# Kernel tuning notes

Hardware: AMD Instinct MI355X
Metric: run time of the kernel (lower is better)

Reference implementation:

```python
import jax, jax.numpy as jnp
import numpy as np

NUM_HEADS = 32
NUM_KV_HEADS = 8
HEAD_DIM = 128
SCALE = 0.08838834764831845  # head_dim ** -0.5
LENS = [1024, 900, 800, 700, 600, 500, 400, 300]  # ragged sequence lengths


def setup_inputs() -> dict:
    key = jax.random.key(0)
    kq, kk, kv = jax.random.split(key, 3)
    cu = np.concatenate([[0], np.cumsum(LENS)]).astype(np.int32)
    T = int(cu[-1])  # 5224 total tokens
    q = jax.random.normal(kq, (T, NUM_HEADS * HEAD_DIM), jnp.float32)
    k = jax.random.normal(kk, (T, NUM_KV_HEADS * HEAD_DIM), jnp.float32)
    v = jax.random.normal(kv, (T, NUM_KV_HEADS * HEAD_DIM), jnp.float32)
    return {"q": q, "k": k, "v": v, "cu_seqlens": jnp.asarray(cu), "max_seqlen": 1024}


def _varlen_indices(cu_seqlens, total_tokens):
    # For each flat token, which sequence it belongs to and its position within it.
    pos = jnp.arange(total_tokens)
    seq_idx = jnp.searchsorted(cu_seqlens[1:], pos, side='right')
    pos_idx = pos - cu_seqlens[seq_idx]
    return seq_idx, pos_idx


def reference(q, k, v, cu_seqlens, max_seqlen):
    T = q.shape[0]
    B = cu_seqlens.shape[0] - 1
    q = q.reshape(T, NUM_HEADS, HEAD_DIM)
    k = k.reshape(T, NUM_KV_HEADS, HEAD_DIM)
    v = v.reshape(T, NUM_KV_HEADS, HEAD_DIM)
    si, pi = _varlen_indices(cu_seqlens, T)

    # varlen -> padded [B, L, H, D] (scatter)
    def pad(x):
        return jnp.zeros((B, max_seqlen) + x.shape[1:], x.dtype).at[si, pi].set(x)

    qp, kp, vp = pad(q), pad(k), pad(v)

    # GQA: repeat_interleave KV heads to match query heads
    rep = NUM_HEADS // NUM_KV_HEADS
    kp = jnp.repeat(kp, rep, axis=2)
    vp = jnp.repeat(vp, rep, axis=2)

    # causal SDPA on padded tensors
    scores = jnp.einsum('bihd,bjhd->bhij', qp, kp) * SCALE  # [B,H,L,L]
    causal = jnp.tril(jnp.ones((max_seqlen, max_seqlen), bool))
    scores = jnp.where(causal, scores, -jnp.inf)
    attn = jax.nn.softmax(scores, axis=-1)
    op = jnp.einsum('bhij,bjhd->bihd', attn, vp)  # [B,L,H,D]

    # padded -> varlen [T, H, D] (gather)
    return op[si, pi]
```

## Files before the change

### kernel.cpp

```cpp
#include <hip/hip_runtime.h>
#include <math.h>

#define NUM_HEADS 32
#define NUM_KV_HEADS 8
#define HEAD_DIM 128
#define QSTRIDE 4096
#define KSTRIDE 1024
#define SCALE 0.08838834764831845f
#define BM 128
#define PSP 72
#define K1C (SCALE * 1.4426950408889634f)
#define K2C (6.0f * 1.4426950408889634f)

typedef __attribute__((ext_vector_type(8))) short short8;
typedef __attribute__((ext_vector_type(16))) float floatx16;
typedef __attribute__((ext_vector_type(4))) float f32x4;

__constant__ unsigned char PERM41[41] = {
  7, 15, 6, 14, 21, 5, 13, 20, 26, 31, 4, 12, 19, 25, 35, 30,
  3, 11, 18, 24, 34, 38, 29, 2, 10, 17, 23, 33, 37, 40, 28,
  1, 9, 16, 22, 32, 36, 39, 27, 0, 8};

__device__ __forceinline__ ushort f2bf(float f) {
  union { float f; unsigned u; } x; x.f = f;
  unsigned r = x.u + 0x7fffu + ((x.u >> 16) & 1u);
  return (ushort)(r >> 16);
}

__device__ __forceinline__ unsigned cvtpk(float lo, float hi) {
  unsigned r;
  asm("v_cvt_pk_bf16_f32 %0, %1, %2" : "=v"(r) : "v"(lo), "v"(hi));
  return r;
}

__global__ __launch_bounds__(256)
void prep(const float* __restrict__ k, const float* __restrict__ v,
          ushort* __restrict__ kfr, ushort* __restrict__ vfr,
          int T, int NB32, int NB16) {
  const int kt = (int)blockIdx.x * 64;
  const int kvh = (int)blockIdx.y;
  __shared__ __align__(16) ushort Kt[64][136];
  __shared__ __align__(16) ushort Vs[128][PSP];
  {
    const int key = threadIdx.x >> 2;
    const int dc = (threadIdx.x & 3) * 32;
    const bool inb = (kt + key) < T;
    const float* gk = k + (size_t)(kt + key) * KSTRIDE + kvh * HEAD_DIM + dc;
    const float* gv = v + (size_t)(kt + key) * KSTRIDE + kvh * HEAD_DIM + dc;
    #pragma unroll
    for (int i = 0; i < 32; i += 8) {
      float4 a = inb ? *(const float4*)(gk + i) : make_float4(0.f, 0.f, 0.f, 0.f);
      float4 b = inb ? *(const float4*)(gk + i + 4) : make_float4(0.f, 0.f, 0.f, 0.f);
      ushort w[8] = {f2bf(a.x), f2bf(a.y), f2bf(a.z), f2bf(a.w),
                     f2bf(b.x), f2bf(b.y), f2bf(b.z), f2bf(b.w)};
      *(short8*)&Kt[key][dc + i] = *(short8*)w;
    }
    #pragma unroll
    for (int i = 0; i < 32; i += 4) {
      float4 x = inb ? *(const float4*)(gv + i) : make_float4(0.f, 0.f, 0.f, 0.f);
      Vs[dc + i + 0][key] = f2bf(x.x);
      Vs[dc + i + 1][key] = f2bf(x.y);
      Vs[dc + i + 2][key] = f2bf(x.z);
      Vs[dc + i + 3][key] = f2bf(x.w);
    }
  }
  __syncthreads();
  const int l = threadIdx.x & 63;
  const int wv = threadIdx.x >> 6;
  const int l32 = l & 31;
  const int hb = l >> 5;
  #pragma unroll
  for (int q0 = 0; q0 < 4; q0++) {
    int c = q0 * 4 + wv;
    int kb2 = c >> 3, s = c & 7;
    short8 d = *(const short8*)&Kt[kb2 * 32 + l32][s * 16 + hb * 8];
    *(short8*)(kfr + ((size_t)(kvh * NB32 + (kt >> 5) + kb2) * 8 + s) * 512 + l * 8) = d;
  }
  #pragma unroll
  for (int q0 = 0; q0 < 4; q0++) {
    int c = q0 * 4 + wv;
    int kb = c >> 2, i = c & 3;
    short8 d = *(const short8*)&Vs[i * 32 + l32][kb * 16 + hb * 8];
    *(short8*)(vfr + ((size_t)(kvh * NB16 + (kt >> 4) + kb) * 4 + i) * 512 + l * 8) = d;
  }
}

__global__ __launch_bounds__(256, 2)
void fa_kernel(const float* __restrict__ q, const ushort* __restrict__ kfr,
               const ushort* __restrict__ vfr, const int* __restrict__ cu,
               float* __restrict__ out, int T, int NB32, int NB16, int B, int nt) {
  const int tid = threadIdx.x;
  const int wave = tid >> 6;
  const int lane = tid & 63;
  const int l32 = lane & 31;
  const int half = lane >> 5;
  const int h = ((int)blockIdx.x & 7) * 4 + ((int)blockIdx.x >> 3);
  const int kvh = h >> 2;
  const int tile = (nt == 41) ? (int)PERM41[blockIdx.y] : (nt - 1 - (int)blockIdx.y);
  const int row0 = tile * BM;
  const int wrow0 = row0 + wave * 32;
  const int myrow = wrow0 + l32;

  int rs_q = 0, tk_q = -1;
  if (myrow < T) {
    int s = 0;
    while (s < B - 1 && cu[s + 1] <= myrow) s++;
    rs_q = cu[s]; tk_q = myrow;
  }
  const int wkt0 = (__shfl(rs_q, 0, 64) / 32) * 32;
  const int wtmax = (wrow0 < T) ? min(wrow0 + 31, T - 1) : -1;

  short8 aq[8];
  if (myrow < T) {
    const float* gq = q + (size_t)myrow * QSTRIDE + h * HEAD_DIM + half * 8;
    #pragma unroll
    for (int s = 0; s < 8; s++) {
      f32x4 x = __builtin_nontemporal_load((const f32x4*)(gq + s * 16));
      f32x4 y = __builtin_nontemporal_load((const f32x4*)(gq + s * 16 + 4));
      ushort w[8] = {f2bf(x.x), f2bf(x.y), f2bf(x.z), f2bf(x.w),
                     f2bf(y.x), f2bf(y.y), f2bf(y.z), f2bf(y.w)};
      aq[s] = *(short8*)w;
    }
  } else {
    #pragma unroll
    for (int s = 0; s < 8; s++) aq[s] = (short8){0, 0, 0, 0, 0, 0, 0, 0};
  }

  const ushort* kp = kfr + (size_t)kvh * NB32 * 4096 + (size_t)(wkt0 >> 5) * 4096 + lane * 8;
  const ushort* vp = vfr + (size_t)kvh * NB16 * 2048 + (size_t)(wkt0 >> 4) * 2048 + lane * 8;

  short8 kf[8], vf[8];
  #pragma unroll
  for (int s = 0; s < 8; s++) kf[s] = *(const short8*)(kp + s * 512);
  #pragma unroll
  for (int c = 0; c < 8; c++) vf[c] = *(const short8*)(vp + c * 512);

  floatx16 o0 = {0.f,0.f,0.f,0.f,0.f,0.f,0.f,0.f,0.f,0.f,0.f,0.f,0.f,0.f,0.f,0.f};
  floatx16 o1 = o0, o2 = o0, o3 = o0;
  float sm = 0.f;

  for (int kt = wkt0; kt <= wtmax; kt += 32) {
    floatx16 ca = {0.f,0.f,0.f,0.f,0.f,0.f,0.f,0.f,0.f,0.f,0.f,0.f,0.f,0.f,0.f,0.f};
    floatx16 cb = ca;
    __builtin_amdgcn_s_setprio(1);
    #pragma unroll
    for (int s = 0; s < 8; s += 2) {
      ca = __builtin_amdgcn_mfma_f32_32x32x16_bf16(kf[s], aq[s], ca, 0, 0, 0);
      cb = __builtin_amdgcn_mfma_f32_32x32x16_bf16(kf[s + 1], aq[s + 1], cb, 0, 0, 0);
    }
    __builtin_amdgcn_s_setprio(0);

    const bool more = (kt + 32) <= wtmax;
    kp += more ? 4096 : 0;
    #pragma unroll
    for (int s = 0; s < 8; s++) kf[s] = *(const short8*)(kp + s * 512);

    const bool fullt = __all((rs_q <= kt) & (tk_q >= kt + 31));
    if (fullt) {
      #pragma unroll
      for (int r = 0; r < 16; r++) {
        ca[r] = __builtin_amdgcn_exp2f(fmaf(ca[r] + cb[r], K1C, -K2C));
        sm += ca[r];
      }
    } else {
      #pragma unroll
      for (int r = 0; r < 16; r++) {
        int key = kt + (r & 3) + 8 * (r >> 2) + 4 * half;
        bool vld = (key >= rs_q) & (key <= tk_q);
        ca[r] = vld ? __builtin_amdgcn_exp2f(fmaf(ca[r] + cb[r], K1C, -K2C)) : 0.f;
        sm += ca[r];
      }
    }

    #pragma unroll
    for (int g = 0; g < 2; g++) {
      const int r0 = g * 8;
      unsigned w0 = cvtpk(ca[r0 + 0], ca[r0 + 1]);
      unsigned w1 = cvtpk(ca[r0 + 2], ca[r0 + 3]);
      unsigned w2 = cvtpk(ca[r0 + 4], ca[r0 + 5]);
      unsigned w3 = cvtpk(ca[r0 + 6], ca[r0 + 7]);
      asm("v_permlane32_swap_b32 %0, %1" : "+v"(w0), "+v"(w2));
      asm("v_permlane32_swap_b32 %0, %1" : "+v"(w1), "+v"(w3));
      union { unsigned u[4]; short8 s8; } ap;
      ap.u[0] = w0; ap.u[1] = w1; ap.u[2] = w2; ap.u[3] = w3;
      o0 = __builtin_amdgcn_mfma_f32_32x32x16_bf16(ap.s8, vf[g * 4 + 0], o0, 0, 0, 0);
      o1 = __builtin_amdgcn_mfma_f32_32x32x16_bf16(ap.s8, vf[g * 4 + 1], o1, 0, 0, 0);
      o2 = __builtin_amdgcn_mfma_f32_32x32x16_bf16(ap.s8, vf[g * 4 + 2], o2, 0, 0, 0);
      o3 = __builtin_amdgcn_mfma_f32_32x32x16_bf16(ap.s8, vf[g * 4 + 3], o3, 0, 0, 0);
    }

    vp += more ? 4096 : 0;
    #pragma unroll
    for (int c = 0; c < 8; c++) vf[c] = *(const short8*)(vp + c * 512);
  }

  float smT = sm + __shfl_xor(sm, 32, 64);
  #pragma unroll
  for (int r = 0; r < 16; r++) {
    int qr = (r & 3) + 8 * (r >> 2) + 4 * half;
    float dn = __shfl(smT, qr, 64);
    int tkr = __shfl(tk_q, qr, 64);
    if (tkr >= 0) {
      float inv = 1.f / dn;
      float* go = out + (size_t)tkr * QSTRIDE + h * HEAD_DIM + l32;
      __builtin_nontemporal_store(o0[r] * inv, go);
      __builtin_nontemporal_store(o1[r] * inv, go + 32);
      __builtin_nontemporal_store(o2[r] * inv, go + 64);
      __builtin_nontemporal_store(o3[r] * inv, go + 96);
    }
  }
}

extern "C" void kernel_launch(void* const* d_in, const int* in_sizes, int n_in,
                              void* d_out, int out_size, void* d_ws, size_t ws_size,
                              hipStream_t stream) {
  const float* q = (const float*)d_in[0];
  const float* k = (const float*)d_in[1];
  const float* v = (const float*)d_in[2];
  const int* cu = (const int*)d_in[3];
  float* out = (float*)d_out;
  int T = in_sizes[0] / QSTRIDE;
  int B = in_sizes[3] - 1;
  int Tpad = ((T + 63) / 64) * 64;
  int NB32 = Tpad / 32, NB16 = Tpad / 16;

  ushort* kfr = (ushort*)d_ws;
  ushort* vfr = kfr + (size_t)Tpad * 1024;

  hipLaunchKernelGGL(prep, dim3(Tpad / 64, NUM_KV_HEADS), dim3(256), 0, stream,
                     k, v, kfr, vfr, T, NB32, NB16);
  int nt = (T + BM - 1) / BM;
  hipLaunchKernelGGL(fa_kernel, dim3(NUM_HEADS, nt), dim3(256), 0, stream,
                     q, kfr, vfr, cu, out, T, NB32, NB16, B, nt);
}
```

Before: 246.8 us.

## Switch attention to 16x16x32 MFMA with 64-row query tiles

Replaces the 32x32x16 MFMA tiling with 16x16x32 instructions, so each wave now handles 16 query rows instead of 32 and each block covers 64 rows. The prep kernel is rewritten to emit K and V fragments in the matching layout, and the P matrix is rearranged using permlane32 and permlane16 swaps. The smaller tiles double the grid, reduce causal work wasted on the diagonal and cut register use, which allows three blocks per CU. In exchange, each K/V fragment is reused across fewer query rows, so more K/V data is loaded overall.

Measured after the change: 257.9 us. +4.5%, slower.

```diff
diff --git a/kernel.cpp b/kernel.cpp
--- a/kernel.cpp
+++ b/kernel.cpp
@@ -7,13 +7,11 @@
 #define QSTRIDE 4096
 #define KSTRIDE 1024
 #define SCALE 0.08838834764831845f
-#define BM 128
 #define PSP 72
 #define K1C (SCALE * 1.4426950408889634f)
 #define K2C (6.0f * 1.4426950408889634f)
 
 typedef __attribute__((ext_vector_type(8))) short short8;
-typedef __attribute__((ext_vector_type(16))) float floatx16;
 typedef __attribute__((ext_vector_type(4))) float f32x4;
 
 __constant__ unsigned char PERM41[41] = {
@@ -67,39 +65,40 @@
   __syncthreads();
   const int l = threadIdx.x & 63;
   const int wv = threadIdx.x >> 6;
-  const int l32 = l & 31;
-  const int hb = l >> 5;
+  const int c16 = l & 15;
+  const int g4 = l >> 4;
   #pragma unroll
   for (int q0 = 0; q0 < 4; q0++) {
     int c = q0 * 4 + wv;
-    int kb2 = c >> 3, s = c & 7;
-    short8 d = *(const short8*)&Kt[kb2 * 32 + l32][s * 16 + hb * 8];
-    *(short8*)(kfr + ((size_t)(kvh * NB32 + (kt >> 5) + kb2) * 8 + s) * 512 + l * 8) = d;
+    int kb = c >> 2, ks = c & 3;
+    short8 d = *(const short8*)&Kt[kb * 16 + c16][ks * 32 + g4 * 8];
+    *(short8*)(kfr + ((size_t)(kvh * NB16 + (kt >> 4) + kb) * 4 + ks) * 512 + l * 8) = d;
   }
   #pragma unroll
   for (int q0 = 0; q0 < 4; q0++) {
     int c = q0 * 4 + wv;
-    int kb = c >> 2, i = c & 3;
-    short8 d = *(const short8*)&Vs[i * 32 + l32][kb * 16 + hb * 8];
-    *(short8*)(vfr + ((size_t)(kvh * NB16 + (kt >> 4) + kb) * 4 + i) * 512 + l * 8) = d;
-  }
-}
-
-__global__ __launch_bounds__(256, 2)
+    int kb = c >> 3, dt = c & 7;
+    short8 d = *(const short8*)&Vs[dt * 16 + c16][kb * 32 + g4 * 8];
+    *(short8*)(vfr + ((size_t)(kvh * NB32 + (kt >> 5) + kb) * 8 + dt) * 512 + l * 8) = d;
+  }
+}
+
+__global__ __launch_bounds__(256, 3)
 void fa_kernel(const float* __restrict__ q, const ushort* __restrict__ kfr,
                const ushort* __restrict__ vfr, const int* __restrict__ cu,
                float* __restrict__ out, int T, int NB32, int NB16, int B, int nt) {
   const int tid = threadIdx.x;
   const int wave = tid >> 6;
   const int lane = tid & 63;
-  const int l32 = lane & 31;
-  const int half = lane >> 5;
+  const int c16 = lane & 15;
+  const int g4 = lane >> 4;
   const int h = ((int)blockIdx.x & 7) * 4 + ((int)blockIdx.x >> 3);
   const int kvh = h >> 2;
-  const int tile = (nt == 41) ? (int)PERM41[blockIdx.y] : (nt - 1 - (int)blockIdx.y);
-  const int row0 = tile * BM;
-  const int wrow0 = row0 + wave * 32;
-  const int myrow = wrow0 + l32;
+  const int by = (int)blockIdx.y;
+  const int tile = (nt == 82) ? ((int)PERM41[by >> 1] * 2 + 1 - (by & 1))
+                              : (nt - 1 - by);
+  const int wrow0 = tile * 64 + wave * 16;
+  const int myrow = wrow0 + c16;
 
   int rs_q = 0, tk_q = -1;
   if (myrow < T) {
@@ -108,105 +107,107 @@
     rs_q = cu[s]; tk_q = myrow;
   }
   const int wkt0 = (__shfl(rs_q, 0, 64) / 32) * 32;
-  const int wtmax = (wrow0 < T) ? min(wrow0 + 31, T - 1) : -1;
-
-  short8 aq[8];
+  const int wtmax = (wrow0 < T) ? min(wrow0 + 15, T - 1) : -1;
+
+  short8 aq[4];
   if (myrow < T) {
-    const float* gq = q + (size_t)myrow * QSTRIDE + h * HEAD_DIM + half * 8;
-    #pragma unroll
-    for (int s = 0; s < 8; s++) {
-      f32x4 x = __builtin_nontemporal_load((const f32x4*)(gq + s * 16));
-      f32x4 y = __builtin_nontemporal_load((const f32x4*)(gq + s * 16 + 4));
+    const float* gq = q + (size_t)myrow * QSTRIDE + h * HEAD_DIM + g4 * 8;
+    #pragma unroll
+    for (int ks = 0; ks < 4; ks++) {
+      f32x4 x = __builtin_nontemporal_load((const f32x4*)(gq + ks * 32));
+      f32x4 y = __builtin_nontemporal_load((const f32x4*)(gq + ks * 32 + 4));
       ushort w[8] = {f2bf(x.x), f2bf(x.y), f2bf(x.z), f2bf(x.w),
                      f2bf(y.x), f2bf(y.y), f2bf(y.z), f2bf(y.w)};
-      aq[s] = *(short8*)w;
+      aq[ks] = *(short8*)w;
     }
   } else {
     #pragma unroll
-    for (int s = 0; s < 8; s++) aq[s] = (short8){0, 0, 0, 0, 0, 0, 0, 0};
-  }
-
-  const ushort* kp = kfr + (size_t)kvh * NB32 * 4096 + (size_t)(wkt0 >> 5) * 4096 + lane * 8;
-  const ushort* vp = vfr + (size_t)kvh * NB16 * 2048 + (size_t)(wkt0 >> 4) * 2048 + lane * 8;
+    for (int ks = 0; ks < 4; ks++) aq[ks] = (short8){0, 0, 0, 0, 0, 0, 0, 0};
+  }
+
+  const ushort* kp = kfr + ((size_t)(kvh * NB16 + (wkt0 >> 4)) * 4) * 512 + lane * 8;
+  const ushort* vp = vfr + ((size_t)(kvh * NB32 + (wkt0 >> 5)) * 8) * 512 + lane * 8;
 
   short8 kf[8], vf[8];
   #pragma unroll
-  for (int s = 0; s < 8; s++) kf[s] = *(const short8*)(kp + s * 512);
-  #pragma unroll
-  for (int c = 0; c < 8; c++) vf[c] = *(const short8*)(vp + c * 512);
-
-  floatx16 o0 = {0.f,0.f,0.f,0.f,0.f,0.f,0.f,0.f,0.f,0.f,0.f,0.f,0.f,0.f,0.f,0.f};
-  floatx16 o1 = o0, o2 = o0, o3 = o0;
+  for (int i = 0; i < 8; i++) kf[i] = *(const short8*)(kp + i * 512);
+  #pragma unroll
+  for (int i = 0; i < 8; i++) vf[i] = *(const short8*)(vp + i * 512);
+
+  f32x4 o[8];
+  #pragma unroll
+  for (int dt = 0; dt < 8; dt++) o[dt] = (f32x4){0.f, 0.f, 0.f, 0.f};
   float sm = 0.f;
 
   for (int kt = wkt0; kt <= wtmax; kt += 32) {
-    floatx16 ca = {0.f,0.f,0.f,0.f,0.f,0.f,0.f,0.f,0.f,0.f,0.f,0.f,0.f,0.f,0.f,0.f};
-    floatx16 cb = ca;
+    f32x4 ca = {0.f, 0.f, 0.f, 0.f};
+    f32x4 cb = ca;
     __builtin_amdgcn_s_setprio(1);
     #pragma unroll
-    for (int s = 0; s < 8; s += 2) {
-      ca = __builtin_amdgcn_mfma_f32_32x32x16_bf16(kf[s], aq[s], ca, 0, 0, 0);
-      cb = __builtin_amdgcn_mfma_f32_32x32x16_bf16(kf[s + 1], aq[s + 1], cb, 0, 0, 0);
+    for (int ks = 0; ks < 4; ks++) {
+      ca = __builtin_amdgcn_mfma_f32_16x16x32_bf16(kf[ks], aq[ks], ca, 0, 0, 0);
+      cb = __builtin_amdgcn_mfma_f32_16x16x32_bf16(kf[4 + ks], aq[ks], cb, 0, 0, 0);
     }
     __builtin_amdgcn_s_setprio(0);
 
     const bool more = (kt + 32) <= wtmax;
     kp += more ? 4096 : 0;
     #pragma unroll
-    for (int s = 0; s < 8; s++) kf[s] = *(const short8*)(kp + s * 512);
+    for (int i = 0; i < 8; i++) kf[i] = *(const short8*)(kp + i * 512);
 
     const bool fullt = __all((rs_q <= kt) & (tk_q >= kt + 31));
     if (fullt) {
       #pragma unroll
-      for (int r = 0; r < 16; r++) {
-        ca[r] = __builtin_amdgcn_exp2f(fmaf(ca[r] + cb[r], K1C, -K2C));
-        sm += ca[r];
+      for (int r = 0; r < 4; r++) {
+        ca[r] = __builtin_amdgcn_exp2f(fmaf(ca[r], K1C, -K2C));
+        cb[r] = __builtin_amdgcn_exp2f(fmaf(cb[r], K1C, -K2C));
+        sm += ca[r] + cb[r];
       }
     } else {
       #pragma unroll
-      for (int r = 0; r < 16; r++) {
-        int key = kt + (r & 3) + 8 * (r >> 2) + 4 * half;
-        bool vld = (key >= rs_q) & (key <= tk_q);
-        ca[r] = vld ? __builtin_amdgcn_exp2f(fmaf(ca[r] + cb[r], K1C, -K2C)) : 0.f;
-        sm += ca[r];
+      for (int r = 0; r < 4; r++) {
+        int key = kt + 4 * g4 + r;
+        bool v0 = (key >= rs_q) & (key <= tk_q);
+        bool v1 = ((key + 16) >= rs_q) & ((key + 16) <= tk_q);
+        ca[r] = v0 ? __builtin_amdgcn_exp2f(fmaf(ca[r], K1C, -K2C)) : 0.f;
+        cb[r] = v1 ? __builtin_amdgcn_exp2f(fmaf(cb[r], K1C, -K2C)) : 0.f;
+        sm += ca[r] + cb[r];
       }
     }
 
-    #pragma unroll
-    for (int g = 0; g < 2; g++) {
-      const int r0 = g * 8;
-      unsigned w0 = cvtpk(ca[r0 + 0], ca[r0 + 1]);
-      unsigned w1 = cvtpk(ca[r0 + 2], ca[r0 + 3]);
-      unsigned w2 = cvtpk(ca[r0 + 4], ca[r0 + 5]);
-      unsigned w3 = cvtpk(ca[r0 + 6], ca[r0 + 7]);
-      asm("v_permlane32_swap_b32 %0, %1" : "+v"(w0), "+v"(w2));
-      asm("v_permlane32_swap_b32 %0, %1" : "+v"(w1), "+v"(w3));
-      union { unsigned u[4]; short8 s8; } ap;
-      ap.u[0] = w0; ap.u[1] = w1; ap.u[2] = w2; ap.u[3] = w3;
-      o0 = __builtin_amdgcn_mfma_f32_32x32x16_bf16(ap.s8, vf[g * 4 + 0], o0, 0, 0, 0);
-      o1 = __builtin_amdgcn_mfma_f32_32x32x16_bf16(ap.s8, vf[g * 4 + 1], o1, 0, 0, 0);
-      o2 = __builtin_amdgcn_mfma_f32_32x32x16_bf16(ap.s8, vf[g * 4 + 2], o2, 0, 0, 0);
-      o3 = __builtin_amdgcn_mfma_f32_32x32x16_bf16(ap.s8, vf[g * 4 + 3], o3, 0, 0, 0);
-    }
+    unsigned u0 = cvtpk(ca[0], ca[1]);
+    unsigned u1 = cvtpk(ca[2], ca[3]);
+    unsigned v0 = cvtpk(cb[0], cb[1]);
+    unsigned v1 = cvtpk(cb[2], cb[3]);
+    asm("v_permlane32_swap_b32 %0, %1" : "+v"(u0), "+v"(v0));
+    asm("v_permlane32_swap_b32 %0, %1" : "+v"(u1), "+v"(v1));
+    asm("v_permlane16_swap_b32 %0, %1" : "+v"(u0), "+v"(v0));
+    asm("v_permlane16_swap_b32 %0, %1" : "+v"(u1), "+v"(v1));
+    union { unsigned u[4]; short8 s8; } ap;
+    ap.u[0] = u0; ap.u[1] = u1; ap.u[2] = v0; ap.u[3] = v1;
+
+    #pragma unroll
+    for (int dt = 0; dt < 8; dt++)
+      o[dt] = __builtin_amdgcn_mfma_f32_16x16x32_bf16(ap.s8, vf[dt], o[dt], 0, 0, 0);
 
     vp += more ? 4096 : 0;
     #pragma unroll
-    for (int c = 0; c < 8; c++) vf[c] = *(const short8*)(vp + c * 512);
-  }
-
-  float smT = sm + __shfl_xor(sm, 32, 64);
-  #pragma unroll
-  for (int r = 0; r < 16; r++) {
-    int qr = (r & 3) + 8 * (r >> 2) + 4 * half;
+    for (int i = 0; i < 8; i++) vf[i] = *(const short8*)(vp + i * 512);
+  }
+
+  float t1 = sm + __shfl_xor(sm, 16, 64);
+  float smT = t1 + __shfl_xor(t1, 32, 64);
+  #pragma unroll
+  for (int r = 0; r < 4; r++) {
+    int qr = 4 * g4 + r;
     float dn = __shfl(smT, qr, 64);
     int tkr = __shfl(tk_q, qr, 64);
     if (tkr >= 0) {
       float inv = 1.f / dn;
-      float* go = out + (size_t)tkr * QSTRIDE + h * HEAD_DIM + l32;
-      __builtin_nontemporal_store(o0[r] * inv, go);
-      __builtin_nontemporal_store(o1[r] * inv, go + 32);
-      __builtin_nontemporal_store(o2[r] * inv, go + 64);
-      __builtin_nontemporal_store(o3[r] * inv, go + 96);
+      float* go = out + (size_t)tkr * QSTRIDE + h * HEAD_DIM + c16;
+      #pragma unroll
+      for (int dt = 0; dt < 8; dt++)
+        __builtin_nontemporal_store(o[dt][r] * inv, go + dt * 16);
     }
   }
 }
@@ -229,7 +230,7 @@
 
   hipLaunchKernelGGL(prep, dim3(Tpad / 64, NUM_KV_HEADS), dim3(256), 0, stream,
                      k, v, kfr, vfr, T, NB32, NB16);
-  int nt = (T + BM - 1) / BM;
-  hipLaunchKernelGGL(fa_kernel, dim3(NUM_HEADS, nt), dim3(256), 0, stream,
-                     q, kfr, vfr, cu, out, T, NB32, NB16, B, nt);
-}
+  int nt64 = (T + 63) / 64;
+  hipLaunchKernelGGL(fa_kernel, dim3(NUM_HEADS, nt64), dim3(256), 0, stream,
+                     q, kfr, vfr, cu, out, T, NB32, NB16, B, nt64);
+}
```
